# Optimization experiments

Hardware: AMD Instinct MI355X
Metric: run time of the kernel (lower is better)

## Reference

```python
import jax, jax.numpy as jnp
import numpy as np

D_MODEL = 768
N_HEADS = 12
HEAD = D_MODEL // N_HEADS  # 64


def setup_inputs() -> dict:
    key = jax.random.key(0)
    ks = jax.random.split(key, 10)
    s = 1.0 / np.sqrt(D_MODEL)
    x = jax.random.normal(ks[0], (4, 2048, D_MODEL), dtype=jnp.float32)
    # per-head projection weights stacked: [H, D, head]
    Wq = jax.random.normal(ks[1], (N_HEADS, D_MODEL, HEAD), dtype=jnp.float32) * s
    bq = jax.random.normal(ks[2], (N_HEADS, HEAD), dtype=jnp.float32) * 0.01
    Wk = jax.random.normal(ks[3], (N_HEADS, D_MODEL, HEAD), dtype=jnp.float32) * s
    bk = jax.random.normal(ks[4], (N_HEADS, HEAD), dtype=jnp.float32) * 0.01
    Wv = jax.random.normal(ks[5], (N_HEADS, D_MODEL, HEAD), dtype=jnp.float32) * s
    bv = jax.random.normal(ks[6], (N_HEADS, HEAD), dtype=jnp.float32) * 0.01
    Wo = jax.random.normal(ks[7], (D_MODEL, D_MODEL), dtype=jnp.float32) * s
    bo = jax.random.normal(ks[8], (D_MODEL,), dtype=jnp.float32) * 0.01
    return {"x": x, "Wq": Wq, "bq": bq, "Wk": Wk, "bk": bk,
            "Wv": Wv, "bv": bv, "Wo": Wo, "bo": bo}


def reference(x, Wq, bq, Wk, bk, Wv, bv, Wo, bo):
    # x: [B,S,D]; per-head projections fused over the head axis.
    q = jnp.einsum('bsd,hde->bhse', x, Wq) + bq[None, :, None, :]
    k = jnp.einsum('bsd,hde->bhse', x, Wk) + bk[None, :, None, :]
    v = jnp.einsum('bsd,hde->bhse', x, Wv) + bv[None, :, None, :]
    scale = 1.0 / jnp.sqrt(jnp.asarray(HEAD, dtype=x.dtype))
    scores = jnp.einsum('bhqe,bhke->bhqk', q, k) * scale  # [B,H,S,S]
    attn = jax.nn.softmax(scores, axis=-1)
    out = jnp.einsum('bhqk,bhke->bhqe', attn, v)  # [B,H,S,head]
    B, H, S, E = out.shape
    # concat heads (head order 0..H-1 along last dim)
    out = out.transpose(0, 2, 1, 3).reshape(B, S, H * E)
    return out @ Wo + bo
```

## Files before the change

### kernel.cpp

```cpp
#include <hip/hip_runtime.h>

typedef __bf16 bf16x8 __attribute__((ext_vector_type(8)));
typedef __bf16 bf16x4 __attribute__((ext_vector_type(4)));
typedef float f32x4 __attribute__((ext_vector_type(4)));

#define QSCALE 0.18033688011112042f

__device__ __forceinline__ void gload16(const void* g, void* l) {
  __builtin_amdgcn_global_load_lds((const __attribute__((address_space(1))) void*)g,
                                   (__attribute__((address_space(3))) void*)l, 16, 0, 0);
}

__device__ __forceinline__ float fexp2(float x) {
#if __has_builtin(__builtin_amdgcn_exp2f)
  return __builtin_amdgcn_exp2f(x);
#else
  return exp2f(x);
#endif
}

__device__ __forceinline__ f32x4 mfma16(bf16x8 a, bf16x8 b, f32x4 c) {
  return __builtin_amdgcn_mfma_f32_16x16x32_bf16(a, b, c, 0, 0, 0);
}

__device__ __forceinline__ unsigned pkbf(float a, float b) {
  union { __bf16 h[2]; unsigned u; } t;
  t.h[0] = (__bf16)a; t.h[1] = (__bf16)b;
  return t.u;
}

__device__ __forceinline__ void pl16swap(unsigned& a, unsigned& b, int g) {
#if __has_builtin(__builtin_amdgcn_permlane16_swap)
  auto r = __builtin_amdgcn_permlane16_swap(a, b, false, false);
  a = r[0]; b = r[1];
#else
  unsigned as_ = (unsigned)__shfl_xor((int)a, 16, 64);
  unsigned bs_ = (unsigned)__shfl_xor((int)b, 16, 64);
  bool odd = g & 1;
  unsigned an = odd ? bs_ : a;
  unsigned bn = odd ? b : as_;
  a = an; b = bn;
#endif
}

__global__ __launch_bounds__(256) void k_cvt_x(const float4* __restrict__ x,
                                               bf16x4* __restrict__ xb) {
  int i = blockIdx.x * 256 + threadIdx.x;
  float4 v = x[i];
  bf16x4 o;
  o[0] = (__bf16)v.x; o[1] = (__bf16)v.y; o[2] = (__bf16)v.z; o[3] = (__bf16)v.w;
  xb[i] = o;
}

__global__ __launch_bounds__(256) void k_cvt_wqkv(
    const float* __restrict__ Wq, const float* __restrict__ Wk,
    const float* __restrict__ Wv, const float* __restrict__ bq,
    const float* __restrict__ bk, const float* __restrict__ bv,
    __bf16* __restrict__ Wt, float* __restrict__ bias) {
  int g = blockIdx.x * 256 + threadIdx.x;
  int n = g / 192;
  int d4 = g - n * 192;
  int d = d4 * 4;
  int t = n / 768;
  int rr = n - t * 768;
  int h = rr >> 6, e = rr & 63;
  const float* W = (t == 0) ? Wq : ((t == 1) ? Wk : Wv);
  const float* bs = (t == 0) ? bq : ((t == 1) ? bk : bv);
  bf16x4 o;
#pragma unroll
  for (int i = 0; i < 4; ++i) o[i] = (__bf16)W[(size_t)(h * 768 + d + i) * 64 + e];
  *(bf16x4*)(Wt + (size_t)n * 768 + d) = o;
  if (d4 == 0) bias[n] = bs[h * 64 + e];
}

__global__ __launch_bounds__(256) void k_cvt_wo(const float* __restrict__ Wo,
                                                __bf16* __restrict__ Wt) {
  int g = blockIdx.x * 256 + threadIdx.x;
  int n = g / 192;
  int d4 = g - n * 192;
  int d = d4 * 4;
  bf16x4 o;
#pragma unroll
  for (int i = 0; i < 4; ++i) o[i] = (__bf16)Wo[(size_t)(d + i) * 768 + n];
  *(bf16x4*)(Wt + (size_t)n * 768 + d) = o;
}

template <int MODE>
__global__ __launch_bounds__(256, 2) void k_gemm(
    const __bf16* __restrict__ A, const __bf16* __restrict__ Bt,
    const float* __restrict__ bias, __bf16* __restrict__ Qd,
    __bf16* __restrict__ Kd, __bf16* __restrict__ VTd,
    float* __restrict__ outF) {
  constexpr int KD = 768;
  __shared__ __bf16 As[2][128 * 64];
  __shared__ __bf16 Bs[2][128 * 64];
  const int tid = threadIdx.x, lane = tid & 63, wid = tid >> 6;
  const int wr = wid >> 1, wc = wid & 1;
  const int bm = blockIdx.x, bn = blockIdx.y;
  const f32x4 z4 = {0.f, 0.f, 0.f, 0.f};
  f32x4 acc[4][4];
#pragma unroll
  for (int a = 0; a < 4; ++a)
#pragma unroll
    for (int b = 0; b < 4; ++b) acc[a][b] = z4;

  const char* Ab = (const char*)A + (size_t)bm * 128 * (KD * 2);
  const char* Bb = (const char*)Bt + (size_t)bn * 128 * (KD * 2);

  auto stage = [&](int kb, int buf) {
#pragma unroll
    for (int i = 0; i < 4; ++i) {
      int o = (wid * 4 + i) * 1024 + lane * 16;
      int row = o >> 7;
      int col = (o & 127) ^ ((row & 7) << 4);
      gload16(Ab + (size_t)row * (KD * 2) + kb * 128 + col,
              (char*)As[buf] + (wid * 4 + i) * 1024);
      gload16(Bb + (size_t)row * (KD * 2) + kb * 128 + col,
              (char*)Bs[buf] + (wid * 4 + i) * 1024);
    }
  };

  stage(0, 0);

  for (int kb = 0; kb < KD / 64; ++kb) {
    const int cur = kb & 1;
    if (kb < KD / 64 - 1) {
      stage(kb + 1, cur ^ 1);
      asm volatile("s_waitcnt vmcnt(8)" ::: "memory");
    } else {
      asm volatile("s_waitcnt vmcnt(0)" ::: "memory");
    }
    __builtin_amdgcn_s_barrier();
#pragma unroll
    for (int ks = 0; ks < 2; ++ks) {
      bf16x8 af[4], bfr[4];
#pragma unroll
      for (int ar = 0; ar < 4; ++ar) {
        int rl = wr * 64 + ar * 16 + (lane & 15);
        int byt = rl * 128 + ((ks * 64 + (lane >> 4) * 16) ^ ((rl & 7) << 4));
        af[ar] = *(const bf16x8*)((const char*)As[cur] + byt);
      }
#pragma unroll
      for (int bc = 0; bc < 4; ++bc) {
        int rl = wc * 64 + bc * 16 + (lane & 15);
        int byt = rl * 128 + ((ks * 64 + (lane >> 4) * 16) ^ ((rl & 7) << 4));
        bfr[bc] = *(const bf16x8*)((const char*)Bs[cur] + byt);
      }
#pragma unroll
      for (int ar = 0; ar < 4; ++ar)
#pragma unroll
        for (int bc = 0; bc < 4; ++bc)
          acc[ar][bc] = mfma16(af[ar], bfr[bc], acc[ar][bc]);
    }
    __builtin_amdgcn_s_barrier();
  }

#pragma unroll
  for (int ar = 0; ar < 4; ++ar) {
#pragma unroll
    for (int bc = 0; bc < 4; ++bc) {
      int n = bn * 128 + wc * 64 + bc * 16 + (lane & 15);
      float bval = bias[n];
#pragma unroll
      for (int r = 0; r < 4; ++r) {
        int m = bm * 128 + wr * 64 + ar * 16 + (lane >> 4) * 4 + r;
        float val = acc[ar][bc][r] + bval;
        if constexpr (MODE == 0) {
          int t = n / 768;
          int rr = n - t * 768;
          int h = rr >> 6, e = rr & 63;
          int b = m >> 11, s = m & 2047;
          size_t bh = (size_t)(b * 12 + h);
          if (t == 0)
            Qd[(bh * 2048 + s) * 64 + e] = (__bf16)(val * QSCALE);
          else if (t == 1)
            Kd[(bh * 2048 + s) * 64 + e] = (__bf16)val;
          else
            VTd[(bh * 64 + e) * 2048 + s] = (__bf16)val;
        } else {
          outF[(size_t)m * 768 + n] = val;
        }
      }
    }
  }
}

__global__ __launch_bounds__(256, 3) void k_attn(const __bf16* __restrict__ Qg,
                                                 const __bf16* __restrict__ Kg,
                                                 const __bf16* __restrict__ Vg,
                                                 __bf16* __restrict__ AO) {
  constexpr int S = 2048;
  constexpr int NT = S / 64;
  __shared__ __bf16 Ks[3][64 * 64];
  __shared__ __bf16 Vs[3][64 * 64];
  const int tid = threadIdx.x, lane = tid & 63, wid = tid >> 6;
  const int q = lane & 15, g = lane >> 4;
  const int q7s = (q & 7) << 4;
  const int vg = ((g & 1) << 5) | ((g >> 1) << 4);
  const int lin = blockIdx.x + blockIdx.y * 16;
  const int xcd = lin & 7, pos = lin >> 3;
  const int bh = xcd * 6 + (pos >> 4);
  const int qt = pos & 15;
  const int bb = bh / 12, hh = bh - bb * 12;
  const size_t hoff = (size_t)bh * S * 64;
  const int q0 = qt * 128 + wid * 32;

  bf16x8 qb[2][2];
#pragma unroll
  for (int rt = 0; rt < 2; ++rt)
#pragma unroll
    for (int ks = 0; ks < 2; ++ks)
      qb[rt][ks] = *(const bf16x8*)(Qg + hoff + (size_t)(q0 + rt * 16 + q) * 64 +
                                    ks * 32 + g * 8);

  const f32x4 z4 = {0.f, 0.f, 0.f, 0.f};
  f32x4 acc[2][4];
#pragma unroll
  for (int a = 0; a < 2; ++a)
#pragma unroll
    for (int b = 0; b < 4; ++b) acc[a][b] = z4;
  float l_p[2] = {0.f, 0.f};

  const char* Kb = (const char*)(Kg + hoff);
  const char* Vb = (const char*)(Vg + (size_t)bh * 64 * S);

  auto stage = [&](int kv, int buf) {
#pragma unroll
    for (int i = 0; i < 2; ++i) {
      int o = (wid * 2 + i) * 1024 + lane * 16;
      int row = o >> 7;
      int col = (o & 127) ^ ((row & 7) << 4);
      gload16(Kb + (size_t)(kv * 64 + row) * 128 + col,
              (char*)Ks[buf] + (wid * 2 + i) * 1024);
      gload16(Vb + (size_t)row * (S * 2) + (size_t)kv * 128 + col,
              (char*)Vs[buf] + (wid * 2 + i) * 1024);
    }
  };

  auto qk = [&](const char* Kc, f32x4 (&sa)[4][2]) {
#pragma unroll
    for (int ct = 0; ct < 4; ++ct) {
      sa[ct][0] = z4;
      sa[ct][1] = z4;
    }
    __builtin_amdgcn_s_setprio(1);
#pragma unroll
    for (int ks = 0; ks < 2; ++ks)
#pragma unroll
      for (int ct = 0; ct < 4; ++ct) {
        int rl = ct * 16 + q;
        bf16x8 ka = *(const bf16x8*)(Kc + rl * 128 + ((ks * 64 + g * 16) ^ q7s));
        sa[ct][0] = mfma16(ka, qb[0][ks], sa[ct][0]);
        sa[ct][1] = mfma16(ka, qb[1][ks], sa[ct][1]);
      }
    __builtin_amdgcn_s_setprio(0);
  };

  stage(0, 0);
  stage(1, 1);
  asm volatile("s_waitcnt vmcnt(4)" ::: "memory");
  __builtin_amdgcn_s_barrier();

  f32x4 sa[4][2];
  qk((const char*)Ks[0], sa);

  for (int kv = 0; kv < NT; ++kv) {
    if (kv < NT - 2) stage(kv + 2, (kv + 2) % 3);
    const char* Vc = (const char*)Vs[kv % 3];

    bf16x8 vf[2][4];
#pragma unroll
    for (int ks = 0; ks < 2; ++ks)
#pragma unroll
      for (int et = 0; et < 4; ++et) {
        int rl = et * 16 + q;
        vf[ks][et] = *(const bf16x8*)(Vc + rl * 128 + ((ks * 64 + vg) ^ q7s));
      }

    bf16x8 pb[2][2];
#pragma unroll
    for (int rt = 0; rt < 2; ++rt) {
      float sum = 0.f;
      unsigned w[4][2];
#pragma unroll
      for (int ct = 0; ct < 4; ++ct) {
        float p0 = fexp2(sa[ct][rt][0]);
        float p1 = fexp2(sa[ct][rt][1]);
        float p2 = fexp2(sa[ct][rt][2]);
        float p3 = fexp2(sa[ct][rt][3]);
        sum += (p0 + p1) + (p2 + p3);
        w[ct][0] = pkbf(p0, p1);
        w[ct][1] = pkbf(p2, p3);
      }
      l_p[rt] += sum;
      pl16swap(w[0][0], w[1][0], g);
      pl16swap(w[0][1], w[1][1], g);
      pl16swap(w[2][0], w[3][0], g);
      pl16swap(w[2][1], w[3][1], g);
      union { unsigned u[4]; bf16x8 v; } f0, f1;
      f0.u[0] = w[0][0]; f0.u[1] = w[0][1]; f0.u[2] = w[1][0]; f0.u[3] = w[1][1];
      f1.u[0] = w[2][0]; f1.u[1] = w[2][1]; f1.u[2] = w[3][0]; f1.u[3] = w[3][1];
      pb[rt][0] = f0.v;
      pb[rt][1] = f1.v;
    }

    if (kv < NT - 1) {
      if (kv < NT - 2) {
        asm volatile("s_waitcnt vmcnt(4)" ::: "memory");
      } else {
        asm volatile("s_waitcnt vmcnt(0)" ::: "memory");
      }
      __builtin_amdgcn_s_barrier();
      qk((const char*)Ks[(kv + 1) % 3], sa);
    }

    __builtin_amdgcn_s_setprio(1);
#pragma unroll
    for (int ks = 0; ks < 2; ++ks)
#pragma unroll
      for (int et = 0; et < 4; ++et) {
        acc[0][et] = mfma16(vf[ks][et], pb[0][ks], acc[0][et]);
        acc[1][et] = mfma16(vf[ks][et], pb[1][ks], acc[1][et]);
      }
    __builtin_amdgcn_s_setprio(0);
  }

#pragma unroll
  for (int rt = 0; rt < 2; ++rt) {
    float l = l_p[rt];
    l += __shfl_xor(l, 16, 64);
    l += __shfl_xor(l, 32, 64);
    float inv = 1.0f / l;
    int srow = q0 + rt * 16 + q;
#pragma unroll
    for (int et = 0; et < 4; ++et) {
      bf16x4 ov;
#pragma unroll
      for (int r = 0; r < 4; ++r) ov[r] = (__bf16)(acc[rt][et][r] * inv);
      *(bf16x4*)(AO + ((size_t)bb * S + srow) * 768 + hh * 64 + et * 16 + g * 4) =
          ov;
    }
  }
}

extern "C" void kernel_launch(void* const* d_in, const int* in_sizes, int n_in,
                              void* d_out, int out_size, void* d_ws,
                              size_t ws_size, hipStream_t stream) {
  const float* x = (const float*)d_in[0];
  const float* Wq = (const float*)d_in[1];
  const float* bq = (const float*)d_in[2];
  const float* Wk = (const float*)d_in[3];
  const float* bk = (const float*)d_in[4];
  const float* Wv = (const float*)d_in[5];
  const float* bv = (const float*)d_in[6];
  const float* Wo = (const float*)d_in[7];
  const float* bo = (const float*)d_in[8];
  float* out = (float*)d_out;
  char* ws = (char*)d_ws;

  __bf16* xb = (__bf16*)(ws + 0);
  __bf16* wqkv = (__bf16*)(ws + 12582912);
  __bf16* wot = (__bf16*)(ws + 16121856);
  float* biasq = (float*)(ws + 17301504);
  __bf16* Qb = (__bf16*)(ws + 17310720);
  __bf16* Kb = (__bf16*)(ws + 29893632);
  __bf16* VT = (__bf16*)(ws + 42476544);

  k_cvt_x<<<6144, 256, 0, stream>>>((const float4*)x, (bf16x4*)xb);
  k_cvt_wqkv<<<1728, 256, 0, stream>>>(Wq, Wk, Wv, bq, bk, bv, wqkv, biasq);
  k_cvt_wo<<<576, 256, 0, stream>>>(Wo, wot);
  k_gemm<0><<<dim3(64, 18), 256, 0, stream>>>(xb, wqkv, biasq, Qb, Kb, VT,
                                              nullptr);
  k_attn<<<dim3(16, 48), 256, 0, stream>>>(Qb, Kb, VT, xb );
  k_gemm<1><<<dim3(64, 6), 256, 0, stream>>>(xb, wot, bo, nullptr, nullptr,
                                             nullptr, out);
}
```

Measured before the change: 161.4 us.

## Split attention KV columns across waves with LDS cross-wave reduction

Each block now handles 64 query rows instead of 128. Within a KV tile, each of the four waves takes a 16-key slice for all 64 rows, instead of each wave owning 32 query rows over the full tile. P·V uses 16x16x16 MFMAs, which drops the permlane swap. Partial accumulators and row sums are reduced across waves through LDS in a serialized four-step loop before one wave writes the output. This doubles the grid and removes the permutes, at the cost of more, smaller MFMAs and a barrier-heavy epilogue reduction.

```diff
diff --git a/kernel.cpp b/kernel.cpp
--- a/kernel.cpp
+++ b/kernel.cpp
@@ -3,6 +3,7 @@
 typedef __bf16 bf16x8 __attribute__((ext_vector_type(8)));
 typedef __bf16 bf16x4 __attribute__((ext_vector_type(4)));
 typedef float f32x4 __attribute__((ext_vector_type(4)));
+typedef short s16x4 __attribute__((ext_vector_type(4)));
 
 #define QSCALE 0.18033688011112042f
 
@@ -23,24 +24,27 @@
   return __builtin_amdgcn_mfma_f32_16x16x32_bf16(a, b, c, 0, 0, 0);
 }
 
+__device__ __forceinline__ f32x4 mfma16k16(bf16x4 a, bf16x4 b, f32x4 c) {
+#if __has_builtin(__builtin_amdgcn_mfma_f32_16x16x16_bf16)
+  return __builtin_amdgcn_mfma_f32_16x16x16_bf16(a, b, c, 0, 0, 0);
+#elif __has_builtin(__builtin_amdgcn_mfma_f32_16x16x16bf16_1k)
+  union { bf16x4 h; s16x4 s; } ua, ub;
+  ua.h = a; ub.h = b;
+  return __builtin_amdgcn_mfma_f32_16x16x16bf16_1k(ua.s, ub.s, c, 0, 0, 0);
+#else
+  union { bf16x4 q[2]; bf16x8 v; } a8, b8;
+  a8.q[0] = a; a8.q[1] = a;
+  bf16x4 z;
+  z[0] = (__bf16)0.f; z[1] = (__bf16)0.f; z[2] = (__bf16)0.f; z[3] = (__bf16)0.f;
+  b8.q[0] = b; b8.q[1] = z;
+  return __builtin_amdgcn_mfma_f32_16x16x32_bf16(a8.v, b8.v, c, 0, 0, 0);
+#endif
+}
+
 __device__ __forceinline__ unsigned pkbf(float a, float b) {
   union { __bf16 h[2]; unsigned u; } t;
   t.h[0] = (__bf16)a; t.h[1] = (__bf16)b;
   return t.u;
-}
-
-__device__ __forceinline__ void pl16swap(unsigned& a, unsigned& b, int g) {
-#if __has_builtin(__builtin_amdgcn_permlane16_swap)
-  auto r = __builtin_amdgcn_permlane16_swap(a, b, false, false);
-  a = r[0]; b = r[1];
-#else
-  unsigned as_ = (unsigned)__shfl_xor((int)a, 16, 64);
-  unsigned bs_ = (unsigned)__shfl_xor((int)b, 16, 64);
-  bool odd = g & 1;
-  unsigned an = odd ? bs_ : a;
-  unsigned bn = odd ? b : as_;
-  a = an; b = bn;
-#endif
 }
 
 __global__ __launch_bounds__(256) void k_cvt_x(const float4* __restrict__ x,
@@ -196,30 +200,29 @@
   const int tid = threadIdx.x, lane = tid & 63, wid = tid >> 6;
   const int q = lane & 15, g = lane >> 4;
   const int q7s = (q & 7) << 4;
-  const int vg = ((g & 1) << 5) | ((g >> 1) << 4);
-  const int lin = blockIdx.x + blockIdx.y * 16;
+  const int lin = blockIdx.x + blockIdx.y * 32;
   const int xcd = lin & 7, pos = lin >> 3;
-  const int bh = xcd * 6 + (pos >> 4);
-  const int qt = pos & 15;
+  const int bh = xcd * 6 + (pos >> 5);
+  const int qt = pos & 31;
   const int bb = bh / 12, hh = bh - bb * 12;
   const size_t hoff = (size_t)bh * S * 64;
-  const int q0 = qt * 128 + wid * 32;
-
-  bf16x8 qb[2][2];
-#pragma unroll
-  for (int rt = 0; rt < 2; ++rt)
+  const int q0 = qt * 64;
+
+  bf16x8 qb[4][2];
+#pragma unroll
+  for (int rt = 0; rt < 4; ++rt)
 #pragma unroll
     for (int ks = 0; ks < 2; ++ks)
       qb[rt][ks] = *(const bf16x8*)(Qg + hoff + (size_t)(q0 + rt * 16 + q) * 64 +
                                     ks * 32 + g * 8);
 
   const f32x4 z4 = {0.f, 0.f, 0.f, 0.f};
-  f32x4 acc[2][4];
-#pragma unroll
-  for (int a = 0; a < 2; ++a)
+  f32x4 acc[4][4];
+#pragma unroll
+  for (int a = 0; a < 4; ++a)
 #pragma unroll
     for (int b = 0; b < 4; ++b) acc[a][b] = z4;
-  float l_p[2] = {0.f, 0.f};
+  float l_p[4] = {0.f, 0.f, 0.f, 0.f};
 
   const char* Kb = (const char*)(Kg + hoff);
   const char* Vb = (const char*)(Vg + (size_t)bh * 64 * S);
@@ -237,22 +240,17 @@
     }
   };
 
-  auto qk = [&](const char* Kc, f32x4 (&sa)[4][2]) {
-#pragma unroll
-    for (int ct = 0; ct < 4; ++ct) {
-      sa[ct][0] = z4;
-      sa[ct][1] = z4;
-    }
+  auto qk = [&](const char* Kc, f32x4 (&sa)[4]) {
+#pragma unroll
+    for (int rt = 0; rt < 4; ++rt) sa[rt] = z4;
+    const int rl = wid * 16 + q;
     __builtin_amdgcn_s_setprio(1);
 #pragma unroll
-    for (int ks = 0; ks < 2; ++ks)
-#pragma unroll
-      for (int ct = 0; ct < 4; ++ct) {
-        int rl = ct * 16 + q;
-        bf16x8 ka = *(const bf16x8*)(Kc + rl * 128 + ((ks * 64 + g * 16) ^ q7s));
-        sa[ct][0] = mfma16(ka, qb[0][ks], sa[ct][0]);
-        sa[ct][1] = mfma16(ka, qb[1][ks], sa[ct][1]);
-      }
+    for (int ks = 0; ks < 2; ++ks) {
+      bf16x8 ka = *(const bf16x8*)(Kc + rl * 128 + ((ks * 64 + g * 16) ^ q7s));
+#pragma unroll
+      for (int rt = 0; rt < 4; ++rt) sa[rt] = mfma16(ka, qb[rt][ks], sa[rt]);
+    }
     __builtin_amdgcn_s_setprio(0);
   };
 
@@ -261,47 +259,35 @@
   asm volatile("s_waitcnt vmcnt(4)" ::: "memory");
   __builtin_amdgcn_s_barrier();
 
-  f32x4 sa[4][2];
+  f32x4 sa[4];
   qk((const char*)Ks[0], sa);
 
+  int bc = 0;
   for (int kv = 0; kv < NT; ++kv) {
-    if (kv < NT - 2) stage(kv + 2, (kv + 2) % 3);
-    const char* Vc = (const char*)Vs[kv % 3];
-
-    bf16x8 vf[2][4];
-#pragma unroll
-    for (int ks = 0; ks < 2; ++ks)
-#pragma unroll
-      for (int et = 0; et < 4; ++et) {
-        int rl = et * 16 + q;
-        vf[ks][et] = *(const bf16x8*)(Vc + rl * 128 + ((ks * 64 + vg) ^ q7s));
-      }
-
-    bf16x8 pb[2][2];
-#pragma unroll
-    for (int rt = 0; rt < 2; ++rt) {
-      float sum = 0.f;
-      unsigned w[4][2];
-#pragma unroll
-      for (int ct = 0; ct < 4; ++ct) {
-        float p0 = fexp2(sa[ct][rt][0]);
-        float p1 = fexp2(sa[ct][rt][1]);
-        float p2 = fexp2(sa[ct][rt][2]);
-        float p3 = fexp2(sa[ct][rt][3]);
-        sum += (p0 + p1) + (p2 + p3);
-        w[ct][0] = pkbf(p0, p1);
-        w[ct][1] = pkbf(p2, p3);
-      }
-      l_p[rt] += sum;
-      pl16swap(w[0][0], w[1][0], g);
-      pl16swap(w[0][1], w[1][1], g);
-      pl16swap(w[2][0], w[3][0], g);
-      pl16swap(w[2][1], w[3][1], g);
-      union { unsigned u[4]; bf16x8 v; } f0, f1;
-      f0.u[0] = w[0][0]; f0.u[1] = w[0][1]; f0.u[2] = w[1][0]; f0.u[3] = w[1][1];
-      f1.u[0] = w[2][0]; f1.u[1] = w[2][1]; f1.u[2] = w[3][0]; f1.u[3] = w[3][1];
-      pb[rt][0] = f0.v;
-      pb[rt][1] = f1.v;
+    const int b1 = (bc == 2) ? 0 : bc + 1;
+    const int b2 = (b1 == 2) ? 0 : b1 + 1;
+    if (kv < NT - 2) stage(kv + 2, b2);
+    const char* Vc = (const char*)Vs[bc];
+
+    bf16x4 vf[4];
+#pragma unroll
+    for (int et = 0; et < 4; ++et) {
+      int rl = et * 16 + q;
+      vf[et] = *(const bf16x4*)(Vc + rl * 128 + ((wid * 32 + g * 8) ^ q7s));
+    }
+
+    bf16x4 pb[4];
+#pragma unroll
+    for (int rt = 0; rt < 4; ++rt) {
+      float p0 = fexp2(sa[rt][0]);
+      float p1 = fexp2(sa[rt][1]);
+      float p2 = fexp2(sa[rt][2]);
+      float p3 = fexp2(sa[rt][3]);
+      l_p[rt] += (p0 + p1) + (p2 + p3);
+      union { unsigned u[2]; bf16x4 v; } f;
+      f.u[0] = pkbf(p0, p1);
+      f.u[1] = pkbf(p2, p3);
+      pb[rt] = f.v;
     }
 
     if (kv < NT - 1) {
@@ -311,34 +297,76 @@
         asm volatile("s_waitcnt vmcnt(0)" ::: "memory");
       }
       __builtin_amdgcn_s_barrier();
-      qk((const char*)Ks[(kv + 1) % 3], sa);
+      qk((const char*)Ks[b1], sa);
     }
 
     __builtin_amdgcn_s_setprio(1);
 #pragma unroll
-    for (int ks = 0; ks < 2; ++ks)
+    for (int rt = 0; rt < 4; ++rt)
+#pragma unroll
+      for (int et = 0; et < 4; ++et)
+        acc[rt][et] = mfma16k16(vf[et], pb[rt], acc[rt][et]);
+    __builtin_amdgcn_s_setprio(0);
+    bc = b1;
+  }
+
+  __builtin_amdgcn_s_barrier();
+  float* R = (float*)&Ks[0][0];
+  float* Rl = R + 64 * 68;
+  float lr[4];
+#pragma unroll
+  for (int rt = 0; rt < 4; ++rt) {
+    float s = l_p[rt];
+    s += __shfl_xor(s, 16, 64);
+    s += __shfl_xor(s, 32, 64);
+    lr[rt] = s;
+  }
+  for (int w2 = 0; w2 < 4; ++w2) {
+    if (wid == w2) {
+      if (w2 == 0) {
+#pragma unroll
+        for (int rt = 0; rt < 4; ++rt) {
+#pragma unroll
+          for (int et = 0; et < 4; ++et)
+            *(f32x4*)&R[(rt * 16 + q) * 68 + et * 16 + g * 4] = acc[rt][et];
+          if (g == 0) Rl[rt * 16 + q] = lr[rt];
+        }
+      } else {
+#pragma unroll
+        for (int rt = 0; rt < 4; ++rt) {
+#pragma unroll
+          for (int et = 0; et < 4; ++et) {
+            int idx = (rt * 16 + q) * 68 + et * 16 + g * 4;
+            f32x4 t = *(f32x4*)&R[idx];
+            t += acc[rt][et];
+            if (w2 < 3)
+              *(f32x4*)&R[idx] = t;
+            else
+              acc[rt][et] = t;
+          }
+          if (w2 < 3) {
+            if (g == 0) Rl[rt * 16 + q] += lr[rt];
+          } else {
+            lr[rt] = Rl[rt * 16 + q] + lr[rt];
+          }
+        }
+      }
+    }
+    __builtin_amdgcn_s_barrier();
+  }
+  if (wid == 3) {
+#pragma unroll
+    for (int rt = 0; rt < 4; ++rt) {
+      float inv = 1.0f / lr[rt];
+      int srow = q0 + rt * 16 + q;
 #pragma unroll
       for (int et = 0; et < 4; ++et) {
-        acc[0][et] = mfma16(vf[ks][et], pb[0][ks], acc[0][et]);
-        acc[1][et] = mfma16(vf[ks][et], pb[1][ks], acc[1][et]);
-      }
-    __builtin_amdgcn_s_setprio(0);
-  }
-
-#pragma unroll
-  for (int rt = 0; rt < 2; ++rt) {
-    float l = l_p[rt];
-    l += __shfl_xor(l, 16, 64);
-    l += __shfl_xor(l, 32, 64);
-    float inv = 1.0f / l;
-    int srow = q0 + rt * 16 + q;
-#pragma unroll
-    for (int et = 0; et < 4; ++et) {
-      bf16x4 ov;
-#pragma unroll
-      for (int r = 0; r < 4; ++r) ov[r] = (__bf16)(acc[rt][et][r] * inv);
-      *(bf16x4*)(AO + ((size_t)bb * S + srow) * 768 + hh * 64 + et * 16 + g * 4) =
-          ov;
+        bf16x4 ov;
+#pragma unroll
+        for (int r = 0; r < 4; ++r) ov[r] = (__bf16)(acc[rt][et][r] * inv);
+        *(bf16x4*)(AO + ((size_t)bb * S + srow) * 768 + hh * 64 + et * 16 +
+                   g * 4) = ov;
+      }
     }
   }
 }
@@ -371,7 +399,7 @@
   k_cvt_wo<<<576, 256, 0, stream>>>(Wo, wot);
   k_gemm<0><<<dim3(64, 18), 256, 0, stream>>>(xb, wqkv, biasq, Qb, Kb, VT,
                                               nullptr);
-  k_attn<<<dim3(16, 48), 256, 0, stream>>>(Qb, Kb, VT, xb );
+  k_attn<<<dim3(32, 48), 256, 0, stream>>>(Qb, Kb, VT, xb );
   k_gemm<1><<<dim3(64, 6), 256, 0, stream>>>(xb, wot, bo, nullptr, nullptr,
                                              nullptr, out);
 }
```

Measured after the change: 175.2 us. 1.09x slower.

## Fuse conversion kernels with tiled LDS transpose and use smaller-tile output GEMM

Applied to the files above, without the earlier changes.

Merges the three fp32-to-bf16 conversion kernels into a single launch. The weight transposes now stage 64x64 tiles through shared memory, giving coalesced reads and 16-byte writes in place of strided per-element gathers. The output projection switches to a new GEMM with 64x128 tiles and a higher occupancy bound, doubling the block count to 768 to fill more compute units. The added shared-memory transpose and smaller tiles reduce operand reuse per block.

```diff
diff --git a/kernel.cpp b/kernel.cpp
--- a/kernel.cpp
+++ b/kernel.cpp
@@ -43,46 +43,69 @@
 #endif
 }
 
-__global__ __launch_bounds__(256) void k_cvt_x(const float4* __restrict__ x,
-                                               bf16x4* __restrict__ xb) {
-  int i = blockIdx.x * 256 + threadIdx.x;
-  float4 v = x[i];
-  bf16x4 o;
-  o[0] = (__bf16)v.x; o[1] = (__bf16)v.y; o[2] = (__bf16)v.z; o[3] = (__bf16)v.w;
-  xb[i] = o;
-}
-
-__global__ __launch_bounds__(256) void k_cvt_wqkv(
+__global__ __launch_bounds__(256) void k_cvt_fused(
     const float* __restrict__ Wq, const float* __restrict__ Wk,
     const float* __restrict__ Wv, const float* __restrict__ bq,
     const float* __restrict__ bk, const float* __restrict__ bv,
-    __bf16* __restrict__ Wt, float* __restrict__ bias) {
-  int g = blockIdx.x * 256 + threadIdx.x;
-  int n = g / 192;
-  int d4 = g - n * 192;
-  int d = d4 * 4;
-  int t = n / 768;
-  int rr = n - t * 768;
-  int h = rr >> 6, e = rr & 63;
-  const float* W = (t == 0) ? Wq : ((t == 1) ? Wk : Wv);
-  const float* bs = (t == 0) ? bq : ((t == 1) ? bk : bv);
-  bf16x4 o;
-#pragma unroll
-  for (int i = 0; i < 4; ++i) o[i] = (__bf16)W[(size_t)(h * 768 + d + i) * 64 + e];
-  *(bf16x4*)(Wt + (size_t)n * 768 + d) = o;
-  if (d4 == 0) bias[n] = bs[h * 64 + e];
-}
-
-__global__ __launch_bounds__(256) void k_cvt_wo(const float* __restrict__ Wo,
-                                                __bf16* __restrict__ Wt) {
-  int g = blockIdx.x * 256 + threadIdx.x;
-  int n = g / 192;
-  int d4 = g - n * 192;
-  int d = d4 * 4;
-  bf16x4 o;
-#pragma unroll
-  for (int i = 0; i < 4; ++i) o[i] = (__bf16)Wo[(size_t)(d + i) * 768 + n];
-  *(bf16x4*)(Wt + (size_t)n * 768 + d) = o;
+    const float* __restrict__ Wo, const float4* __restrict__ x,
+    __bf16* __restrict__ Wt, float* __restrict__ bias,
+    __bf16* __restrict__ Wot, bf16x4* __restrict__ xb) {
+  __shared__ float T[64][68];
+  const int b = blockIdx.x, tid = threadIdx.x;
+  if (b >= 576) {
+    int i = (b - 576) * 256 + tid;
+    float4 v = x[i];
+    bf16x4 o;
+    o[0] = (__bf16)v.x; o[1] = (__bf16)v.y; o[2] = (__bf16)v.z; o[3] = (__bf16)v.w;
+    xb[i] = o;
+    return;
+  }
+  int r0 = tid >> 4, c4 = (tid & 15) * 4;
+  if (b < 432) {
+    int t = b / 144, rem = b - t * 144;
+    int h = rem / 12, dblk = rem - h * 12;
+    const float* W = (t == 0) ? Wq : ((t == 1) ? Wk : Wv);
+#pragma unroll
+    for (int p = 0; p < 4; ++p) {
+      int r = r0 + p * 16;
+      float4 v = *(const float4*)&W[(size_t)(h * 768 + dblk * 64 + r) * 64 + c4];
+      T[r][c4] = v.x; T[r][c4 + 1] = v.y; T[r][c4 + 2] = v.z; T[r][c4 + 3] = v.w;
+    }
+    int outn0 = t * 768 + h * 64;
+    if (dblk == 0 && tid < 64) {
+      const float* bs = (t == 0) ? bq : ((t == 1) ? bk : bv);
+      bias[outn0 + tid] = bs[h * 64 + tid];
+    }
+    __syncthreads();
+    int e = tid >> 2, ch = tid & 3;
+    union { __bf16 h8[8]; bf16x8 v; } u0, u1;
+#pragma unroll
+    for (int j = 0; j < 8; ++j) u0.h8[j] = (__bf16)T[ch * 16 + j][e];
+#pragma unroll
+    for (int j = 0; j < 8; ++j) u1.h8[j] = (__bf16)T[ch * 16 + 8 + j][e];
+    __bf16* dst = Wt + (size_t)(outn0 + e) * 768 + dblk * 64 + ch * 16;
+    *(bf16x8*)dst = u0.v;
+    *(bf16x8*)(dst + 8) = u1.v;
+  } else {
+    int bb = b - 432;
+    int dblk = bb / 12, nblk = bb - dblk * 12;
+#pragma unroll
+    for (int p = 0; p < 4; ++p) {
+      int r = r0 + p * 16;
+      float4 v = *(const float4*)&Wo[(size_t)(dblk * 64 + r) * 768 + nblk * 64 + c4];
+      T[r][c4] = v.x; T[r][c4 + 1] = v.y; T[r][c4 + 2] = v.z; T[r][c4 + 3] = v.w;
+    }
+    __syncthreads();
+    int e = tid >> 2, ch = tid & 3;
+    union { __bf16 h8[8]; bf16x8 v; } u0, u1;
+#pragma unroll
+    for (int j = 0; j < 8; ++j) u0.h8[j] = (__bf16)T[ch * 16 + j][e];
+#pragma unroll
+    for (int j = 0; j < 8; ++j) u1.h8[j] = (__bf16)T[ch * 16 + 8 + j][e];
+    __bf16* dst = Wot + (size_t)(nblk * 64 + e) * 768 + dblk * 64 + ch * 16;
+    *(bf16x8*)dst = u0.v;
+    *(bf16x8*)(dst + 8) = u1.v;
+  }
 }
 
 template <int MODE>
@@ -180,6 +203,95 @@
         } else {
           outF[(size_t)m * 768 + n] = val;
         }
+      }
+    }
+  }
+}
+
+__global__ __launch_bounds__(256, 3) void k_gemm2(
+    const __bf16* __restrict__ A, const __bf16* __restrict__ Bt,
+    const float* __restrict__ bias, float* __restrict__ outF) {
+  constexpr int KD = 768;
+  __shared__ __bf16 As[2][64 * 64];
+  __shared__ __bf16 Bs[2][128 * 64];
+  const int tid = threadIdx.x, lane = tid & 63, wid = tid >> 6;
+  const int q = lane & 15, g = lane >> 4;
+  const int wr = wid >> 1, wc = wid & 1;
+  const int bm = blockIdx.x, bn = blockIdx.y;
+  const f32x4 z4 = {0.f, 0.f, 0.f, 0.f};
+  f32x4 acc[2][4];
+#pragma unroll
+  for (int a = 0; a < 2; ++a)
+#pragma unroll
+    for (int b = 0; b < 4; ++b) acc[a][b] = z4;
+
+  const char* Ab = (const char*)A + (size_t)bm * 64 * (KD * 2);
+  const char* Bb = (const char*)Bt + (size_t)bn * 128 * (KD * 2);
+
+  auto stage = [&](int kb, int buf) {
+#pragma unroll
+    for (int i = 0; i < 2; ++i) {
+      int o = (wid * 2 + i) * 1024 + lane * 16;
+      int row = o >> 7;
+      int col = (o & 127) ^ ((row & 7) << 4);
+      gload16(Ab + (size_t)row * (KD * 2) + kb * 128 + col,
+              (char*)As[buf] + (wid * 2 + i) * 1024);
+    }
+#pragma unroll
+    for (int i = 0; i < 4; ++i) {
+      int o = (wid * 4 + i) * 1024 + lane * 16;
+      int row = o >> 7;
+      int col = (o & 127) ^ ((row & 7) << 4);
+      gload16(Bb + (size_t)row * (KD * 2) + kb * 128 + col,
+              (char*)Bs[buf] + (wid * 4 + i) * 1024);
+    }
+  };
+
+  stage(0, 0);
+
+  for (int kb = 0; kb < KD / 64; ++kb) {
+    const int cur = kb & 1;
+    if (kb < KD / 64 - 1) {
+      stage(kb + 1, cur ^ 1);
+      asm volatile("s_waitcnt vmcnt(6)" ::: "memory");
+    } else {
+      asm volatile("s_waitcnt vmcnt(0)" ::: "memory");
+    }
+    __builtin_amdgcn_s_barrier();
+#pragma unroll
+    for (int ks = 0; ks < 2; ++ks) {
+      bf16x8 af[2], bfr[4];
+#pragma unroll
+      for (int ar = 0; ar < 2; ++ar) {
+        int rl = wr * 32 + ar * 16 + q;
+        int byt = rl * 128 + ((ks * 64 + g * 16) ^ ((rl & 7) << 4));
+        af[ar] = *(const bf16x8*)((const char*)As[cur] + byt);
+      }
+#pragma unroll
+      for (int bc = 0; bc < 4; ++bc) {
+        int rl = wc * 64 + bc * 16 + q;
+        int byt = rl * 128 + ((ks * 64 + g * 16) ^ ((rl & 7) << 4));
+        bfr[bc] = *(const bf16x8*)((const char*)Bs[cur] + byt);
+      }
+#pragma unroll
+      for (int ar = 0; ar < 2; ++ar)
+#pragma unroll
+        for (int bc = 0; bc < 4; ++bc)
+          acc[ar][bc] = mfma16(af[ar], bfr[bc], acc[ar][bc]);
+    }
+    __builtin_amdgcn_s_barrier();
+  }
+
+#pragma unroll
+  for (int ar = 0; ar < 2; ++ar) {
+#pragma unroll
+    for (int bc = 0; bc < 4; ++bc) {
+      int n = bn * 128 + wc * 64 + bc * 16 + q;
+      float bval = bias[n];
+#pragma unroll
+      for (int r = 0; r < 4; ++r) {
+        int m = bm * 64 + wr * 32 + ar * 16 + g * 4 + r;
+        outF[(size_t)m * 768 + n] = acc[ar][bc][r] + bval;
       }
     }
   }
@@ -366,12 +478,11 @@
   __bf16* Kb = (__bf16*)(ws + 29893632);
   __bf16* VT = (__bf16*)(ws + 42476544);
 
-  k_cvt_x<<<6144, 256, 0, stream>>>((const float4*)x, (bf16x4*)xb);
-  k_cvt_wqkv<<<1728, 256, 0, stream>>>(Wq, Wk, Wv, bq, bk, bv, wqkv, biasq);
-  k_cvt_wo<<<576, 256, 0, stream>>>(Wo, wot);
+  k_cvt_fused<<<6720, 256, 0, stream>>>(Wq, Wk, Wv, bq, bk, bv, Wo,
+                                        (const float4*)x, wqkv, biasq, wot,
+                                        (bf16x4*)xb);
   k_gemm<0><<<dim3(64, 18), 256, 0, stream>>>(xb, wqkv, biasq, Qb, Kb, VT,
                                               nullptr);
   k_attn<<<dim3(16, 48), 256, 0, stream>>>(Qb, Kb, VT, xb );
-  k_gemm<1><<<dim3(64, 6), 256, 0, stream>>>(xb, wot, bo, nullptr, nullptr,
-                                             nullptr, out);
-}
+  k_gemm2<<<dim3(128, 6), 256, 0, stream>>>(xb, wot, bo, out);
+}
```

Measured after the change: 148.2 us. -8.2%, faster.
